# Kernel optimization log

Hardware: AMD Instinct MI355X
Metric: run time of the kernel (lower is better)

Reference implementation:

```python
import jax, jax.numpy as jnp
import numpy as np

B, M, N_STYLE, K, F = 4, 8192, 8192, 8, 288


def _graphconv(x, src, dst, W, b, num_nodes):
    # DGL GraphConv, norm='both': h_v = (sum_{u->v} x_u * d_out(u)^-1/2) * d_in(v)^-1/2 @ W + b
    ones = jnp.ones(src.shape[0], x.dtype)
    deg_out = jnp.clip(jax.ops.segment_sum(ones, src, num_segments=num_nodes), 1.0)
    deg_in = jnp.clip(jax.ops.segment_sum(ones, dst, num_segments=num_nodes), 1.0)
    h = x * (deg_out ** -0.5)[:, None]                      # [N, F] src-normalized
    agg = jax.ops.segment_sum(h[src], dst, num_segments=num_nodes)  # gather+scatter-add
    agg = agg * (deg_in ** -0.5)[:, None]
    return agg @ W + b


def setup_inputs() -> dict:
    key = jax.random.key(0)
    ks = jax.random.split(key, 8)
    return {
        "feat_c": jax.random.normal(ks[0], (B, M, F), jnp.float32),
        "feat_s": jax.random.normal(ks[1], (B, N_STYLE, F), jnp.float32),
        "idx_k1": jax.random.randint(ks[2], (B, M, K), 0, N_STYLE, dtype=jnp.int32),
        "idx_k2": jax.random.randint(ks[3], (B, M, K), 0, M, dtype=jnp.int32),
        "W1": jax.random.normal(ks[4], (F, F), jnp.float32) * (1.0 / np.sqrt(F)),
        "b1": jnp.zeros((F,), jnp.float32),
        "W2": jax.random.normal(ks[5], (F, F), jnp.float32) * (1.0 / np.sqrt(F)),
        "b2": jnp.zeros((F,), jnp.float32),
    }


def reference(feat_c, feat_s, idx_k1, idx_k2, W1, b1, W2, b2):
    b, m, f = feat_c.shape
    n = feat_s.shape[1]
    k = idx_k1.shape[2]
    num_nodes = m + n
    # idx_v: range(m).view(1,m,1).expand(2,m,k).view(-1)
    idx_v = jnp.tile(jnp.repeat(jnp.arange(m, dtype=jnp.int32), k), 2)  # [2*m*k]
    # idx_u: cat((idx_k2, idx_k1 + m), dim=1).view(b, -1)
    idx_u = jnp.concatenate([idx_k2, idx_k1 + m], axis=1).reshape(b, -1)  # [b, 2*m*k]
    feat = jnp.concatenate([feat_c, feat_s], axis=1)  # [b, m+n, f]

    def per_graph(x, src):
        h = _graphconv(x, src, idx_v, W1, b1, num_nodes)
        h = jax.nn.relu(h)
        h = _graphconv(h, src, idx_v, W2, b2, num_nodes)
        return h[:m]  # [m, f]

    return jax.vmap(per_graph)(feat, idx_u)  # [b, m, f]
```

## Files before the change

kernel.cpp:

```cpp
#include <hip/hip_runtime.h>

#define B 4
#define M 8192
#define NSTY 8192
#define KNB 8
#define F 288
#define NT (M + NSTY)
#define BM (B * M)
#define SEGL (M * F)

typedef __attribute__((ext_vector_type(8))) short short8;
typedef __attribute__((ext_vector_type(4))) float floatx4;
typedef __attribute__((ext_vector_type(2))) float floatx2;

__device__ __forceinline__ float u2f(unsigned int u) {
    union { unsigned int u; float f; } c; c.u = u; return c.f;
}
__device__ __forceinline__ unsigned short f2b(float x) {
    union { float f; unsigned int u; } c; c.f = x;
    unsigned int r = c.u + 0x7FFFu + ((c.u >> 16) & 1u);
    return (unsigned short)(r >> 16);
}
__device__ __forceinline__ floatx2 bpair(unsigned int p) {
    floatx2 r;
    r.x = u2f(p << 16);
    r.y = u2f(p & 0xFFFF0000u);
    return r;
}
__device__ __forceinline__ void gload_lds16(const void* g, void* l) {
    __builtin_amdgcn_global_load_lds(
        (const __attribute__((address_space(1))) unsigned int*)g,
        (__attribute__((address_space(3))) unsigned int*)l, 16, 0, 0);
}

#define PREP_DEG_BLKS 4
#define PREP_CVT_BLKS 576
#define PREP_PKW_BLKS 162
__global__ __launch_bounds__(1024) void prep_kernel(
                            const int* __restrict__ idx_k1, const int* __restrict__ idx_k2,
                            int* __restrict__ deg,
                            const float* __restrict__ fc, const float* __restrict__ fs,
                            unsigned short* __restrict__ fb,
                            const float* __restrict__ W1, const float* __restrict__ W2,
                            unsigned short* __restrict__ Wp1, unsigned short* __restrict__ Wp2) {
    int blk = blockIdx.x;
    int tid = threadIdx.x;
    if (blk < PREP_DEG_BLKS) {
        __shared__ int h[NT];
        for (int i = tid; i < NT; i += 1024) h[i] = 0;
        __syncthreads();
        int b = blk;
        const int4* p2 = (const int4*)(idx_k2 + (size_t)b * M * KNB);
        const int4* p1 = (const int4*)(idx_k1 + (size_t)b * M * KNB);
        #pragma unroll 2
        for (int i = tid; i < (M * KNB) / 4; i += 1024) {
            int4 v = p2[i];
            atomicAdd(&h[v.x], 1); atomicAdd(&h[v.y], 1);
            atomicAdd(&h[v.z], 1); atomicAdd(&h[v.w], 1);
        }
        #pragma unroll 2
        for (int i = tid; i < (M * KNB) / 4; i += 1024) {
            int4 v = p1[i];
            atomicAdd(&h[M + v.x], 1); atomicAdd(&h[M + v.y], 1);
            atomicAdd(&h[M + v.z], 1); atomicAdd(&h[M + v.w], 1);
        }
        __syncthreads();
        int4* dst = (int4*)(deg + (size_t)b * NT);
        const int4* hs = (const int4*)h;
        for (int i = tid; i < NT / 4; i += 1024) dst[i] = hs[i];
    } else if (blk < PREP_DEG_BLKS + PREP_CVT_BLKS) {
        int cb = blk - PREP_DEG_BLKS;
        int seg = cb / 72;
        int bis = cb - seg * 72;
        int b = seg >> 1, sty = seg & 1;
        const float* src0 = (sty ? fs : fc) + (size_t)b * SEGL;
        unsigned short* dst0 = fb + (size_t)b * 2 * SEGL + (size_t)sty * SEGL;
        unsigned int e0 = (unsigned int)bis * 32768u + (unsigned int)tid * 8u;
        float4 x[8];
        #pragma unroll
        for (int j = 0; j < 4; ++j) {
            const float* s = src0 + e0 + j * 8192u;
            x[2 * j]     = *(const float4*)s;
            x[2 * j + 1] = *(const float4*)(s + 4);
        }
        #pragma unroll
        for (int j = 0; j < 4; ++j) {
            uint4 o;
            o.x = (unsigned int)f2b(x[2*j].x)   | ((unsigned int)f2b(x[2*j].y)   << 16);
            o.y = (unsigned int)f2b(x[2*j].z)   | ((unsigned int)f2b(x[2*j].w)   << 16);
            o.z = (unsigned int)f2b(x[2*j+1].x) | ((unsigned int)f2b(x[2*j+1].y) << 16);
            o.w = (unsigned int)f2b(x[2*j+1].z) | ((unsigned int)f2b(x[2*j+1].w) << 16);
            *(uint4*)(dst0 + e0 + j * 8192u) = o;
        }
    } else {
        int t = (blk - PREP_DEG_BLKS - PREP_CVT_BLKS) * 1024 + tid;
        if (t >= 2 * F * F) return;
        int half = t >= F * F;
        int tt = t - half * F * F;
        int k = tt / F, n = tt - k * F;
        const float* W = half ? W2 : W1;
        unsigned short* Wp = half ? Wp2 : Wp1;
        Wp[((size_t)(k >> 3) * F + n) * 8 + (k & 7)] = f2b(W[tt]);
    }
}

template<int LAYER>
__global__ __launch_bounds__(512, 2) void fused_kernel(
        const unsigned short* __restrict__ src_tbl,
        const int* __restrict__ idx_k1, const int* __restrict__ idx_k2,
        const int* __restrict__ deg,
        const float* __restrict__ bprev,
        const unsigned short* __restrict__ Wp,
        const float* __restrict__ bias,
        void* __restrict__ Cout) {
    const int NK = (LAYER == 1) ? 16 : 8;
    __shared__ __align__(16) unsigned short sA[64 * F];
    __shared__ __align__(16) unsigned short sB[2][4 * F * 8];

    int tid = threadIdx.x;
    int wid = tid >> 6, lane = tid & 63;
    int blk = blockIdx.x;
    int rx = blk & 7;
    int b = rx >> 1;
    int sub = (blk >> 3) * 2 + (rx & 1);
    int rloc = sub * 64;
    int row0 = b * M + rloc;

    if (tid < 128) {
        #pragma unroll
        for (int rr = 0; rr < 9; ++rr)
            gload_lds16(Wp + (rr * 128 + tid) * 8, &sB[0][(rr * 128 + tid) * 8]);
    }

    int i4 = lane >> 4, e = lane & 15;
    const char* baseb = (const char*)(src_tbl + (size_t)b * (size_t)(LAYER == 1 ? NT : M) * F);
    unsigned int lane16 = (unsigned int)lane * 16u;

    float bb[8];
    if (LAYER == 2 && lane < 36) {
        float4 t0 = *(const float4*)(bprev + 8 * lane);
        float4 t1 = *(const float4*)(bprev + 8 * lane + 4);
        bb[0]=fmaxf(t0.x,0.f); bb[1]=fmaxf(t0.y,0.f); bb[2]=fmaxf(t0.z,0.f); bb[3]=fmaxf(t0.w,0.f);
        bb[4]=fmaxf(t1.x,0.f); bb[5]=fmaxf(t1.y,0.f); bb[6]=fmaxf(t1.z,0.f); bb[7]=fmaxf(t1.w,0.f);
    }

    #pragma unroll
    for (int p = 0; p < 2; ++p) {
        int rb = wid * 8 + p * 4;
        size_t eb = ((size_t)b * M + rloc + rb + i4) * KNB;
        int u;
        if (e < 8) u = idx_k2[eb + e];
        else       u = M + idx_k1[eb + e - 8];
        int dg = deg[b * NT + u];
        float w = rsqrtf((float)(dg < 1 ? 1 : dg));
        float wst = (e >= 8) ? w : 0.f;
        unsigned int uoff = (unsigned int)u * (unsigned int)(F * 2);

        #pragma unroll
        for (int i = 0; i < 4; ++i) {
            floatx2 acc[4];
            if (LAYER == 2) {
                float S = 0.f;
                #pragma unroll
                for (int j = 8; j < 16; ++j) S += __shfl(wst, i * 16 + j);
                #pragma unroll
                for (int j = 0; j < 4; ++j) { acc[j].x = bb[2*j] * S; acc[j].y = bb[2*j+1] * S; }
            } else {
                #pragma unroll
                for (int j = 0; j < 4; ++j) acc[j] = (floatx2){0.f, 0.f};
            }

            #pragma unroll
            for (int c = 0; c < NK / 8; ++c) {
                unsigned int off[8];
                #pragma unroll
                for (int k = 0; k < 8; ++k)
                    off[k] = (unsigned int)__shfl((int)uoff, i * 16 + c * 8 + k) + lane16;
                uint4 v[8];
                if (lane < 36) {
                    #pragma unroll
                    for (int k = 0; k < 8; ++k) v[k] = *(const uint4*)(baseb + off[k]);
                }
                #pragma unroll
                for (int k = 0; k < 8; ++k) {
                    float wk = __shfl(w, i * 16 + c * 8 + k);
                    floatx2 wk2 = {wk, wk};
                    acc[0] += wk2 * bpair(v[k].x);
                    acc[1] += wk2 * bpair(v[k].y);
                    acc[2] += wk2 * bpair(v[k].z);
                    acc[3] += wk2 * bpair(v[k].w);
                }
            }

            if (lane < 36) {
                uint4 o;
                o.x = (unsigned int)f2b(acc[0].x*0.25f) | ((unsigned int)f2b(acc[0].y*0.25f) << 16);
                o.y = (unsigned int)f2b(acc[1].x*0.25f) | ((unsigned int)f2b(acc[1].y*0.25f) << 16);
                o.z = (unsigned int)f2b(acc[2].x*0.25f) | ((unsigned int)f2b(acc[2].y*0.25f) << 16);
                o.w = (unsigned int)f2b(acc[3].x*0.25f) | ((unsigned int)f2b(acc[3].y*0.25f) << 16);
                *(uint4*)&sA[(size_t)(rb + i) * F + 8 * lane] = o;
            }
        }
    }

    int wm = wid & 3, wn = wid >> 2;
    int quad = lane >> 4, r16 = lane & 15;

    floatx4 acc9[9];
    #pragma unroll
    for (int ct = 0; ct < 9; ++ct) acc9[ct] = (floatx4){0.f, 0.f, 0.f, 0.f};

    __syncthreads();

    for (int s = 0; s < 9; ++s) {
        if (s < 8 && tid < 128) {
            const unsigned short* srcw = Wp + (size_t)(s + 1) * 4 * F * 8;
            unsigned short* dstb = sB[(s + 1) & 1];
            #pragma unroll
            for (int rr = 0; rr < 9; ++rr)
                gload_lds16(srcw + (rr * 128 + tid) * 8, dstb + (rr * 128 + tid) * 8);
        }
        short8 a0 = *(const short8*)&sA[(wm * 16 + r16) * F + s * 32 + quad * 8];
        const unsigned short* bbp = &sB[s & 1][(quad * F + wn * 144 + r16) * 8];
        #pragma unroll
        for (int ct = 0; ct < 9; ++ct) {
            short8 bf = *(const short8*)(bbp + ct * 128);
            acc9[ct] = __builtin_amdgcn_mfma_f32_16x16x32_bf16(a0, bf, acc9[ct], 0, 0, 0);
        }
        __syncthreads();
    }

    #pragma unroll
    for (int ct = 0; ct < 9; ++ct) {
        int col = wn * 144 + ct * 16 + r16;
        float bc = bias[col];
        #pragma unroll
        for (int rg = 0; rg < 4; ++rg) {
            float v = acc9[ct][rg] + bc;
            if (LAYER == 1) v = fmaxf(v, 0.f);
            int grow = row0 + wm * 16 + quad * 4 + rg;
            if (LAYER == 1) ((unsigned short*)Cout)[(size_t)grow * F + col] = f2b(v);
            else            ((float*)Cout)[(size_t)grow * F + col] = v;
        }
    }
}

extern "C" void kernel_launch(void* const* d_in, const int* in_sizes, int n_in,
                              void* d_out, int out_size, void* d_ws, size_t ws_size,
                              hipStream_t stream) {
    const float* feat_c = (const float*)d_in[0];
    const float* feat_s = (const float*)d_in[1];
    const int*   idx_k1 = (const int*)d_in[2];
    const int*   idx_k2 = (const int*)d_in[3];
    const float* W1     = (const float*)d_in[4];
    const float* b1     = (const float*)d_in[5];
    const float* W2     = (const float*)d_in[6];
    const float* b2     = (const float*)d_in[7];

    char* ws = (char*)d_ws;
    int*            deg  = (int*)ws;
    unsigned short* Wp1  = (unsigned short*)(ws + 262144);
    unsigned short* Wp2  = (unsigned short*)(ws + 262144 + 165888);
    unsigned short* h1b  = (unsigned short*)(ws + 262144 + 2 * 165888);

    unsigned short* featb = (unsigned short*)d_out;
    float*          out   = (float*)d_out;

    prep_kernel<<<PREP_DEG_BLKS + PREP_CVT_BLKS + PREP_PKW_BLKS, 1024, 0, stream>>>(
        idx_k1, idx_k2, deg, feat_c, feat_s, featb, W1, W2, Wp1, Wp2);

    fused_kernel<1><<<BM / 64, 512, 0, stream>>>(
        featb, idx_k1, idx_k2, deg, b1, Wp1, b1, (void*)h1b);

    fused_kernel<2><<<BM / 64, 512, 0, stream>>>(
        h1b, idx_k1, idx_k2, deg, b1, Wp2, b2, (void*)out);
}
```

Measured before the change: 222.7 us.

## Pre-scale gather sources by out-degree norm and software-pipeline neighbor gathers

The source-degree normalization (times 0.25) is folded into the bf16 feature table during the conversion pass and into the layer-1 epilogue, so the gather loop becomes plain sums with no per-neighbor weight shuffles. Because the conversion now needs degrees, prep is split into two launches. The gather loop is restructured into a double-buffered pipeline that issues the next row's loads before consuming the current one. Launch bounds drop to one block per SIMD pair to make room for the extra registers. Costs are an additional kernel launch, possible loss of occupancy, and an extra bf16 rounding step applied after scaling.

```diff
diff --git a/kernel.cpp b/kernel.cpp
--- a/kernel.cpp
+++ b/kernel.cpp
@@ -33,19 +33,16 @@
         (__attribute__((address_space(3))) unsigned int*)l, 16, 0, 0);
 }
 
-#define PREP_DEG_BLKS 4
-#define PREP_CVT_BLKS 576
-#define PREP_PKW_BLKS 162
-__global__ __launch_bounds__(1024) void prep_kernel(
-                            const int* __restrict__ idx_k1, const int* __restrict__ idx_k2,
-                            int* __restrict__ deg,
-                            const float* __restrict__ fc, const float* __restrict__ fs,
-                            unsigned short* __restrict__ fb,
-                            const float* __restrict__ W1, const float* __restrict__ W2,
-                            unsigned short* __restrict__ Wp1, unsigned short* __restrict__ Wp2) {
+#define P0_DEG 4
+#define P0_PKW 162
+__global__ __launch_bounds__(1024) void prep0_kernel(
+        const int* __restrict__ idx_k1, const int* __restrict__ idx_k2,
+        int* __restrict__ deg,
+        const float* __restrict__ W1, const float* __restrict__ W2,
+        unsigned short* __restrict__ Wp1, unsigned short* __restrict__ Wp2) {
     int blk = blockIdx.x;
     int tid = threadIdx.x;
-    if (blk < PREP_DEG_BLKS) {
+    if (blk < P0_DEG) {
         __shared__ int h[NT];
         for (int i = tid; i < NT; i += 1024) h[i] = 0;
         __syncthreads();
@@ -68,32 +65,8 @@
         int4* dst = (int4*)(deg + (size_t)b * NT);
         const int4* hs = (const int4*)h;
         for (int i = tid; i < NT / 4; i += 1024) dst[i] = hs[i];
-    } else if (blk < PREP_DEG_BLKS + PREP_CVT_BLKS) {
-        int cb = blk - PREP_DEG_BLKS;
-        int seg = cb / 72;
-        int bis = cb - seg * 72;
-        int b = seg >> 1, sty = seg & 1;
-        const float* src0 = (sty ? fs : fc) + (size_t)b * SEGL;
-        unsigned short* dst0 = fb + (size_t)b * 2 * SEGL + (size_t)sty * SEGL;
-        unsigned int e0 = (unsigned int)bis * 32768u + (unsigned int)tid * 8u;
-        float4 x[8];
-        #pragma unroll
-        for (int j = 0; j < 4; ++j) {
-            const float* s = src0 + e0 + j * 8192u;
-            x[2 * j]     = *(const float4*)s;
-            x[2 * j + 1] = *(const float4*)(s + 4);
-        }
-        #pragma unroll
-        for (int j = 0; j < 4; ++j) {
-            uint4 o;
-            o.x = (unsigned int)f2b(x[2*j].x)   | ((unsigned int)f2b(x[2*j].y)   << 16);
-            o.y = (unsigned int)f2b(x[2*j].z)   | ((unsigned int)f2b(x[2*j].w)   << 16);
-            o.z = (unsigned int)f2b(x[2*j+1].x) | ((unsigned int)f2b(x[2*j+1].y) << 16);
-            o.w = (unsigned int)f2b(x[2*j+1].z) | ((unsigned int)f2b(x[2*j+1].w) << 16);
-            *(uint4*)(dst0 + e0 + j * 8192u) = o;
-        }
     } else {
-        int t = (blk - PREP_DEG_BLKS - PREP_CVT_BLKS) * 1024 + tid;
+        int t = (blk - P0_DEG) * 1024 + tid;
         if (t >= 2 * F * F) return;
         int half = t >= F * F;
         int tt = t - half * F * F;
@@ -104,8 +77,46 @@
     }
 }
 
+#define P1_BLKS 576
+__global__ __launch_bounds__(1024) void prep1_kernel(
+        const int* __restrict__ deg,
+        const float* __restrict__ fc, const float* __restrict__ fs,
+        unsigned short* __restrict__ fb) {
+    int cb = blockIdx.x;
+    int tid = threadIdx.x;
+    int seg = cb / 72;
+    int bis = cb - seg * 72;
+    int b = seg >> 1, sty = seg & 1;
+    const float* src0 = (sty ? fs : fc) + (size_t)b * SEGL;
+    unsigned short* dst0 = fb + (size_t)b * 2 * SEGL + (size_t)sty * SEGL;
+    unsigned int e0 = (unsigned int)bis * 32768u + (unsigned int)tid * 8u;
+    float4 x[8];
+    #pragma unroll
+    for (int j = 0; j < 4; ++j) {
+        const float* s = src0 + e0 + j * 8192u;
+        x[2 * j]     = *(const float4*)s;
+        x[2 * j + 1] = *(const float4*)(s + 4);
+    }
+    float w[4];
+    #pragma unroll
+    for (int j = 0; j < 4; ++j) {
+        unsigned int row = (e0 + j * 8192u) / 288u;
+        int dg = deg[b * NT + (sty ? M + (int)row : (int)row)];
+        w[j] = 0.25f * rsqrtf((float)(dg < 1 ? 1 : dg));
+    }
+    #pragma unroll
+    for (int j = 0; j < 4; ++j) {
+        uint4 o;
+        o.x = (unsigned int)f2b(x[2*j].x*w[j])   | ((unsigned int)f2b(x[2*j].y*w[j])   << 16);
+        o.y = (unsigned int)f2b(x[2*j].z*w[j])   | ((unsigned int)f2b(x[2*j].w*w[j])   << 16);
+        o.z = (unsigned int)f2b(x[2*j+1].x*w[j]) | ((unsigned int)f2b(x[2*j+1].y*w[j]) << 16);
+        o.w = (unsigned int)f2b(x[2*j+1].z*w[j]) | ((unsigned int)f2b(x[2*j+1].w*w[j]) << 16);
+        *(uint4*)(dst0 + e0 + j * 8192u) = o;
+    }
+}
+
 template<int LAYER>
-__global__ __launch_bounds__(512, 2) void fused_kernel(
+__global__ __launch_bounds__(512, 1) void fused_kernel(
         const unsigned short* __restrict__ src_tbl,
         const int* __restrict__ idx_k1, const int* __restrict__ idx_k2,
         const int* __restrict__ deg,
@@ -114,6 +125,8 @@
         const float* __restrict__ bias,
         void* __restrict__ Cout) {
     const int NK = (LAYER == 1) ? 16 : 8;
+    const int NB = NK / 8;
+    const int TOT = 8 * NB;
     __shared__ __align__(16) unsigned short sA[64 * F];
     __shared__ __align__(16) unsigned short sB[2][4 * F * 8];
 
@@ -133,8 +146,21 @@
     }
 
     int i4 = lane >> 4, e = lane & 15;
-    const char* baseb = (const char*)(src_tbl + (size_t)b * (size_t)(LAYER == 1 ? NT : M) * F);
-    unsigned int lane16 = (unsigned int)lane * 16u;
+    int rw0 = wid * 8;
+    size_t eb0 = ((size_t)b * M + rloc + rw0 + i4) * KNB;
+    size_t eb1 = eb0 + (size_t)4 * KNB;
+    int u0, u1;
+    if (e < 8) { u0 = idx_k2[eb0 + e];     u1 = idx_k2[eb1 + e]; }
+    else       { u0 = M + idx_k1[eb0 + e - 8]; u1 = M + idx_k1[eb1 + e - 8]; }
+    int uoff0 = u0 * (F * 2);
+    int uoff1 = u1 * (F * 2);
+
+    float wst0 = 0.f, wst1 = 0.f;
+    if (LAYER == 2 && e >= 8) {
+        int d0 = deg[b * NT + u0], d1 = deg[b * NT + u1];
+        wst0 = 0.25f * rsqrtf((float)(d0 < 1 ? 1 : d0));
+        wst1 = 0.25f * rsqrtf((float)(d1 < 1 ? 1 : d1));
+    }
 
     float bb[8];
     if (LAYER == 2 && lane < 36) {
@@ -144,64 +170,71 @@
         bb[4]=fmaxf(t1.x,0.f); bb[5]=fmaxf(t1.y,0.f); bb[6]=fmaxf(t1.z,0.f); bb[7]=fmaxf(t1.w,0.f);
     }
 
-    #pragma unroll
-    for (int p = 0; p < 2; ++p) {
-        int rb = wid * 8 + p * 4;
-        size_t eb = ((size_t)b * M + rloc + rb + i4) * KNB;
-        int u;
-        if (e < 8) u = idx_k2[eb + e];
-        else       u = M + idx_k1[eb + e - 8];
-        int dg = deg[b * NT + u];
-        float w = rsqrtf((float)(dg < 1 ? 1 : dg));
-        float wst = (e >= 8) ? w : 0.f;
-        unsigned int uoff = (unsigned int)u * (unsigned int)(F * 2);
-
-        #pragma unroll
-        for (int i = 0; i < 4; ++i) {
-            floatx2 acc[4];
-            if (LAYER == 2) {
-                float S = 0.f;
-                #pragma unroll
-                for (int j = 8; j < 16; ++j) S += __shfl(wst, i * 16 + j);
-                #pragma unroll
-                for (int j = 0; j < 4; ++j) { acc[j].x = bb[2*j] * S; acc[j].y = bb[2*j+1] * S; }
-            } else {
-                #pragma unroll
-                for (int j = 0; j < 4; ++j) acc[j] = (floatx2){0.f, 0.f};
-            }
-
-            #pragma unroll
-            for (int c = 0; c < NK / 8; ++c) {
-                unsigned int off[8];
-                #pragma unroll
-                for (int k = 0; k < 8; ++k)
-                    off[k] = (unsigned int)__shfl((int)uoff, i * 16 + c * 8 + k) + lane16;
-                uint4 v[8];
-                if (lane < 36) {
-                    #pragma unroll
-                    for (int k = 0; k < 8; ++k) v[k] = *(const uint4*)(baseb + off[k]);
-                }
-                #pragma unroll
-                for (int k = 0; k < 8; ++k) {
-                    float wk = __shfl(w, i * 16 + c * 8 + k);
-                    floatx2 wk2 = {wk, wk};
-                    acc[0] += wk2 * bpair(v[k].x);
-                    acc[1] += wk2 * bpair(v[k].y);
-                    acc[2] += wk2 * bpair(v[k].z);
-                    acc[3] += wk2 * bpair(v[k].w);
-                }
-            }
-
-            if (lane < 36) {
-                uint4 o;
-                o.x = (unsigned int)f2b(acc[0].x*0.25f) | ((unsigned int)f2b(acc[0].y*0.25f) << 16);
-                o.y = (unsigned int)f2b(acc[1].x*0.25f) | ((unsigned int)f2b(acc[1].y*0.25f) << 16);
-                o.z = (unsigned int)f2b(acc[2].x*0.25f) | ((unsigned int)f2b(acc[2].y*0.25f) << 16);
-                o.w = (unsigned int)f2b(acc[3].x*0.25f) | ((unsigned int)f2b(acc[3].y*0.25f) << 16);
-                *(uint4*)&sA[(size_t)(rb + i) * F + 8 * lane] = o;
-            }
-        }
-    }
+    const char* baseb = (const char*)(src_tbl + (size_t)b * (size_t)(LAYER == 1 ? NT : M) * F);
+    unsigned int lane16 = (unsigned int)lane * 16u;
+    floatx2 acc[4];
+
+#define MKOFF(OFF, T) do {                                                   \
+        int r_ = (T) / NB, c_ = (T) % NB;                                    \
+        int uo_ = (r_ & 4) ? uoff1 : uoff0;                                  \
+        int sl_ = (r_ & 3) * 16 + c_ * 8;                                    \
+        _Pragma("unroll")                                                    \
+        for (int k_ = 0; k_ < 8; ++k_)                                       \
+            OFF[k_] = (unsigned int)__shfl(uo_, sl_ + k_) + lane16;          \
+    } while (0)
+
+#define LD8(V, OFF) do { if (lane < 36) {                                    \
+        _Pragma("unroll")                                                    \
+        for (int k_ = 0; k_ < 8; ++k_)                                       \
+            V[k_] = *(const uint4*)(baseb + OFF[k_]);                        \
+    } } while (0)
+
+#define CONSUME(V, T) do {                                                   \
+        int r_ = (T) / NB, c_ = (T) % NB;                                    \
+        if (c_ == 0) {                                                       \
+            if (LAYER == 2) {                                                \
+                float ws_ = (r_ & 4) ? wst1 : wst0;                          \
+                float S_ = 0.f;                                              \
+                _Pragma("unroll")                                            \
+                for (int j_ = 8; j_ < 16; ++j_)                              \
+                    S_ += __shfl(ws_, (r_ & 3) * 16 + j_);                   \
+                _Pragma("unroll")                                            \
+                for (int j_ = 0; j_ < 4; ++j_) {                             \
+                    acc[j_].x = bb[2*j_] * S_; acc[j_].y = bb[2*j_+1] * S_;  \
+                }                                                            \
+            } else {                                                         \
+                _Pragma("unroll")                                            \
+                for (int j_ = 0; j_ < 4; ++j_) acc[j_] = (floatx2){0.f,0.f}; \
+            }                                                                \
+        }                                                                    \
+        _Pragma("unroll")                                                    \
+        for (int k_ = 0; k_ < 8; ++k_) {                                     \
+            acc[0] += bpair(V[k_].x); acc[1] += bpair(V[k_].y);              \
+            acc[2] += bpair(V[k_].z); acc[3] += bpair(V[k_].w);              \
+        }                                                                    \
+        if (c_ == NB - 1 && lane < 36) {                                     \
+            uint4 o_;                                                        \
+            o_.x = (unsigned int)f2b(acc[0].x) | ((unsigned int)f2b(acc[0].y) << 16); \
+            o_.y = (unsigned int)f2b(acc[1].x) | ((unsigned int)f2b(acc[1].y) << 16); \
+            o_.z = (unsigned int)f2b(acc[2].x) | ((unsigned int)f2b(acc[2].y) << 16); \
+            o_.w = (unsigned int)f2b(acc[3].x) | ((unsigned int)f2b(acc[3].y) << 16); \
+            *(uint4*)&sA[(size_t)(rw0 + r_) * F + 8 * lane] = o_;            \
+        }                                                                    \
+    } while (0)
+
+    unsigned int offA[8], offB[8];
+    uint4 vA[8], vB[8];
+    MKOFF(offA, 0); LD8(vA, offA);
+    #pragma unroll
+    for (int t = 0; t < TOT; t += 2) {
+        if (t + 1 < TOT) { MKOFF(offB, t + 1); LD8(vB, offB); }
+        CONSUME(vA, t);
+        if (t + 2 < TOT) { MKOFF(offA, t + 2); LD8(vA, offA); }
+        if (t + 1 < TOT) CONSUME(vB, t + 1);
+    }
+#undef MKOFF
+#undef LD8
+#undef CONSUME
 
     int wm = wid & 3, wn = wid >> 2;
     int quad = lane >> 4, r16 = lane & 15;
@@ -230,17 +263,36 @@
         __syncthreads();
     }
 
-    #pragma unroll
-    for (int ct = 0; ct < 9; ++ct) {
-        int col = wn * 144 + ct * 16 + r16;
-        float bc = bias[col];
+    if (LAYER == 1) {
+        int nid = rloc + wm * 16 + quad * 4;
+        int4 dv = *(const int4*)&deg[b * NT + nid];
+        float w4[4];
+        w4[0] = 0.25f * rsqrtf((float)(dv.x < 1 ? 1 : dv.x));
+        w4[1] = 0.25f * rsqrtf((float)(dv.y < 1 ? 1 : dv.y));
+        w4[2] = 0.25f * rsqrtf((float)(dv.z < 1 ? 1 : dv.z));
+        w4[3] = 0.25f * rsqrtf((float)(dv.w < 1 ? 1 : dv.w));
         #pragma unroll
-        for (int rg = 0; rg < 4; ++rg) {
-            float v = acc9[ct][rg] + bc;
-            if (LAYER == 1) v = fmaxf(v, 0.f);
-            int grow = row0 + wm * 16 + quad * 4 + rg;
-            if (LAYER == 1) ((unsigned short*)Cout)[(size_t)grow * F + col] = f2b(v);
-            else            ((float*)Cout)[(size_t)grow * F + col] = v;
+        for (int ct = 0; ct < 9; ++ct) {
+            int col = wn * 144 + ct * 16 + r16;
+            float bc = bias[col];
+            #pragma unroll
+            for (int rg = 0; rg < 4; ++rg) {
+                float v = fmaxf(acc9[ct][rg] + bc, 0.f) * w4[rg];
+                int grow = row0 + wm * 16 + quad * 4 + rg;
+                ((unsigned short*)Cout)[(size_t)grow * F + col] = f2b(v);
+            }
+        }
+    } else {
+        #pragma unroll
+        for (int ct = 0; ct < 9; ++ct) {
+            int col = wn * 144 + ct * 16 + r16;
+            float bc = bias[col];
+            #pragma unroll
+            for (int rg = 0; rg < 4; ++rg) {
+                float v = acc9[ct][rg] + bc;
+                int grow = row0 + wm * 16 + quad * 4 + rg;
+                ((float*)Cout)[(size_t)grow * F + col] = v;
+            }
         }
     }
 }
@@ -266,8 +318,10 @@
     unsigned short* featb = (unsigned short*)d_out;
     float*          out   = (float*)d_out;
 
-    prep_kernel<<<PREP_DEG_BLKS + PREP_CVT_BLKS + PREP_PKW_BLKS, 1024, 0, stream>>>(
-        idx_k1, idx_k2, deg, feat_c, feat_s, featb, W1, W2, Wp1, Wp2);
+    prep0_kernel<<<P0_DEG + P0_PKW, 1024, 0, stream>>>(
+        idx_k1, idx_k2, deg, W1, W2, Wp1, Wp2);
+
+    prep1_kernel<<<P1_BLKS, 1024, 0, stream>>>(deg, feat_c, feat_s, featb);
 
     fused_kernel<1><<<BM / 64, 512, 0, stream>>>(
         featb, idx_k1, idx_k2, deg, b1, Wp1, b1, (void*)h1b);
```

After: 209.6 us. -5.9%, faster.
